# Kernel optimization log

Measured on AMD Instinct MI355X. Metric: run time of the kernel, lower is better.

The kernel has to match this reference:

```python
import jax, jax.numpy as jnp
import numpy as np

EMBED = 768
HEADS = 8
HEAD_DIM = EMBED // HEADS  # 96


def setup_inputs() -> dict:
    key = jax.random.key(0)
    k1, k2, k3, k4, k5 = jax.random.split(key, 5)
    b, n = 4, 2048
    x = jax.random.normal(k1, (b, n, EMBED), dtype=jnp.float32)
    s = 1.0 / np.sqrt(EMBED)
    W_qkv = jax.random.normal(k2, (EMBED, 3 * EMBED), dtype=jnp.float32) * s
    b_qkv = jax.random.normal(k3, (3 * EMBED,), dtype=jnp.float32) * 0.02
    W_proj = jax.random.normal(k4, (EMBED, EMBED), dtype=jnp.float32) * s
    b_proj = jax.random.normal(k5, (EMBED,), dtype=jnp.float32) * 0.02
    return {"x": x, "W_qkv": W_qkv, "b_qkv": b_qkv, "W_proj": W_proj, "b_proj": b_proj}


def reference(x, W_qkv, b_qkv, W_proj, b_proj):
    b, n, _ = x.shape
    qkv = x @ W_qkv + b_qkv  # [b, n, 3*EMBED]
    # rearrange 'b n (h d qkv) -> qkv b h n d': qkv is fastest-varying axis
    qkv = qkv.reshape(b, n, HEADS, HEAD_DIM, 3)
    q = jnp.transpose(qkv[..., 0], (0, 2, 1, 3))  # [b, h, n, d]
    k = jnp.transpose(qkv[..., 1], (0, 2, 1, 3))
    v = jnp.transpose(qkv[..., 2], (0, 2, 1, 3))
    scale = 1.0 / np.sqrt(HEAD_DIM)
    energy = jnp.einsum('bhqd,bhkd->bhqk', q, k) * scale
    attn = jax.nn.softmax(energy, axis=-1)  # dropout p=0 -> identity
    out = jnp.einsum('bhqk,bhkd->bhqd', attn, v)
    out = jnp.transpose(out, (0, 2, 1, 3)).reshape(b, n, EMBED)
    out = out @ W_proj + b_proj
    return out
```

## Files before the change

### kernel.cpp

```cpp
#include <hip/hip_runtime.h>
#include <hip/hip_bf16.h>

#define EMBED 768
#define NHEADS 8
#define HDIM 96
#define SEQ 2048
#define BATCH 4
#define NTOK (BATCH*SEQ)
#define QKVN (3*EMBED)

#define QSCALE 0.14724444f

typedef __attribute__((ext_vector_type(4))) float f32x4;
typedef __attribute__((ext_vector_type(8))) __bf16 bf16x8;

__device__ __forceinline__ unsigned short f2bf(float f) {
  union { float f; unsigned int u; } c; c.f = f;
  unsigned int u = c.u;
  return (unsigned short)((u + 0x7FFFu + ((u >> 16) & 1u)) >> 16);
}

__device__ __forceinline__ unsigned int cvt_pk_bf16(float lo, float hi) {
  unsigned int r;
  asm("v_cvt_pk_bf16_f32 %0, %1, %2" : "=v"(r) : "v"(lo), "v"(hi));
  return r;
}

__device__ __forceinline__ void gload_lds16(const void* g, void* l) {
  __builtin_amdgcn_global_load_lds(
      (const __attribute__((address_space(1))) unsigned int*)g,
      (__attribute__((address_space(3))) unsigned int*)l, 16, 0, 0);
}

__global__ __launch_bounds__(256) void cast_x_kernel(const float4* __restrict__ in,
                                                     ushort4* __restrict__ out, int n4) {
  int i = blockIdx.x * 256 + threadIdx.x;
  if (i >= n4) return;
  float4 v = in[i];
  out[i] = make_ushort4(f2bf(v.x), f2bf(v.y), f2bf(v.z), f2bf(v.w));
}

__global__ __launch_bounds__(256) void transpose_cast_kernel(const float* __restrict__ in,
                                                             unsigned short* __restrict__ out,
                                                             int R, int C, int remap) {
  __shared__ float t[32][33];
  int c0 = blockIdx.x * 32, r0 = blockIdx.y * 32;
  int tx = threadIdx.x & 31, ty = threadIdx.x >> 5;
  #pragma unroll
  for (int i = 0; i < 32; i += 8)
    t[ty + i][tx] = in[(size_t)(r0 + ty + i) * C + c0 + tx];
  __syncthreads();
  #pragma unroll
  for (int i = 0; i < 32; i += 8) {
    int c = c0 + ty + i;
    int rp = remap ? (c % 3) * 768 + c / 3 : c;
    out[(size_t)rp * R + r0 + tx] = f2bf(t[tx][ty + i]);
  }
}

template <int MODE>
__global__ __launch_bounds__(256, 2) void gemm8_kernel(
    const unsigned short* __restrict__ A, const unsigned short* __restrict__ B,
    const float* __restrict__ bias, int K, int NB,
    unsigned short* __restrict__ Qo, unsigned short* __restrict__ Ko,
    unsigned short* __restrict__ Vt, float* __restrict__ out) {
  __shared__ unsigned short As[2][128 * 64];
  __shared__ unsigned short Bs[2][128 * 64];
  const int tid = threadIdx.x;
  const int lane = tid & 63, wid = tid >> 6;
  const int wr = wid >> 1, wc = wid & 1;
  const int l15 = lane & 15, l16 = lane >> 4;
  const int cpx = gridDim.x >> 3;
  const int bid = blockIdx.x;
  const int swz = (bid & 7) * cpx + (bid >> 3);
  const int my = swz / NB, nx = swz - my * NB;
  const int m0 = my * 128, n0 = nx * 128;

  auto stage_half = [&](int buf, int kt, int half) {
    const unsigned short* src = half ? B : A;
    const int base0 = half ? n0 : m0;
    char* dst = (char*)(half ? &Bs[buf][0] : &As[buf][0]);
    #pragma unroll
    for (int i = 0; i < 4; i++) {
      int c = i * 256 + tid;
      int r = c >> 3, s = c & 7;
      gload_lds16(src + (size_t)(base0 + r) * K + kt * 64 + ((s ^ (r & 7)) << 3),
                  dst + (i * 256 + wid * 64) * 16);
    }
  };

  f32x4 acc[4][4] = {};
  const int xr = (l15 & 7) << 4;

  stage_half(0, 0, 0);
  stage_half(0, 0, 1);
  asm volatile("s_waitcnt vmcnt(0)" ::: "memory");
  __builtin_amdgcn_s_barrier();

  const int NT = K >> 6;
  for (int t = 0; t < NT; ++t) {
    const int cur = t & 1;
    const char* Ac = (const char*)&As[cur][0];
    const char* Bc = (const char*)&Bs[cur][0];
    #pragma unroll
    for (int kh = 0; kh < 2; ++kh) {
      bf16x8 af[4], bfr[4];
      #pragma unroll
      for (int mi = 0; mi < 4; mi++)
        af[mi] = *(const bf16x8*)(Ac + (wr * 64 + mi * 16 + l15) * 128 +
                                  ((kh * 64 + l16 * 16) ^ xr));
      #pragma unroll
      for (int ni = 0; ni < 4; ni++)
        bfr[ni] = *(const bf16x8*)(Bc + (wc * 64 + ni * 16 + l15) * 128 +
                                   ((kh * 64 + l16 * 16) ^ xr));
      if (t + 1 < NT) stage_half(cur ^ 1, t + 1, kh);
      __builtin_amdgcn_s_barrier();
      __builtin_amdgcn_s_setprio(1);
      #pragma unroll
      for (int mi = 0; mi < 4; mi++)
        #pragma unroll
        for (int ni = 0; ni < 4; ni++)
          acc[mi][ni] = __builtin_amdgcn_mfma_f32_16x16x32_bf16(af[mi], bfr[ni], acc[mi][ni], 0, 0, 0);
      __builtin_amdgcn_s_setprio(0);
      __builtin_amdgcn_s_barrier();
    }
    asm volatile("s_waitcnt lgkmcnt(0)" ::: "memory");
    asm volatile("s_waitcnt vmcnt(0)" ::: "memory");
    __builtin_amdgcn_sched_barrier(0);
    __builtin_amdgcn_s_barrier();
  }

  if (MODE == 0) {
    #pragma unroll
    for (int mi = 0; mi < 4; mi++) {
      #pragma unroll
      for (int ni = 0; ni < 4; ni++) {
        int base = n0 + wc * 64 + ni * 16;
        int which = base / 768;
        int hd = base - which * 768;
        int h = hd / 96;
        int d0 = hd - h * 96;
        float bb = bias[(hd + l15) * 3 + which];
        int rowb = m0 + wr * 64 + mi * 16 + l16 * 4;
        int bi = rowb >> 11, nnb = rowb & 2047;
        size_t bh = (size_t)(bi * NHEADS + h);
        if (which == 2) {
          int nn2 = (nnb & ~63) | (nnb & 32) | ((nnb & 12) << 1) | ((nnb & 16) >> 2) | (nnb & 3);
          float v0 = acc[mi][ni][0] + bb, v1 = acc[mi][ni][1] + bb;
          float v2 = acc[mi][ni][2] + bb, v3 = acc[mi][ni][3] + bb;
          uint2 pk;
          pk.x = cvt_pk_bf16(v0, v1);
          pk.y = cvt_pk_bf16(v2, v3);
          *(uint2*)(Vt + (bh * HDIM + d0 + l15) * SEQ + nn2) = pk;
        } else {
          #pragma unroll
          for (int j = 0; j < 4; j++) {
            float v = acc[mi][ni][j] + bb;
            int nn = nnb + j;
            if (which == 0) Qo[(bh * SEQ + nn) * HDIM + d0 + l15] = f2bf(v * QSCALE);
            else            Ko[(bh * SEQ + nn) * HDIM + d0 + l15] = f2bf(v);
          }
        }
      }
    }
  } else {
    #pragma unroll
    for (int mi = 0; mi < 4; mi++) {
      #pragma unroll
      for (int ni = 0; ni < 4; ni++) {
        int col = n0 + wc * 64 + ni * 16 + l15;
        float bb = bias[col];
        #pragma unroll
        for (int j = 0; j < 4; j++) {
          int row = m0 + wr * 64 + mi * 16 + l16 * 4 + j;
          out[(size_t)row * EMBED + col] = acc[mi][ni][j] + bb;
        }
      }
    }
  }
}

__global__ __launch_bounds__(512) void attn_kernel(
    const unsigned short* __restrict__ Q, const unsigned short* __restrict__ Kd,
    const unsigned short* __restrict__ Vt, unsigned short* __restrict__ Oa) {
  __shared__ unsigned short Ks[2][64 * 96];
  __shared__ unsigned short Vs[2][96 * 64];

  const int tid = threadIdx.x, lane = tid & 63, wid = tid >> 6;
  const int l15 = lane & 15, l16 = lane >> 4;
  const int bid = blockIdx.x;
  const int swz = (bid & 7) * 64 + (bid >> 3);
  const int qb_ = swz & 15, bh = swz >> 4;
  const int bi = bh >> 3, h = bh & 7;
  const int q0 = qb_ * 128;

  const unsigned short* Qg = Q + ((size_t)bh * SEQ + q0) * HDIM;
  const unsigned short* Kg = Kd + (size_t)bh * SEQ * HDIM;
  const unsigned short* Vg = Vt + (size_t)bh * HDIM * SEQ;

  bf16x8 qf[3];
  #pragma unroll
  for (int ks = 0; ks < 3; ks++)
    qf[ks] = *(const bf16x8*)(Qg + (size_t)(wid * 16 + l15) * HDIM + ks * 32 + l16 * 8);

  auto stageKV = [&](int buf, int k0) {
    gload_lds16(Kg + (size_t)k0 * HDIM + tid * 8, (char*)&Ks[buf][0] + wid * 1024);
    if (wid < 4)
      gload_lds16(Kg + (size_t)k0 * HDIM + (512 + tid) * 8,
                  (char*)&Ks[buf][0] + 8192 + wid * 1024);
    {
      int d = tid >> 3, s = tid & 7;
      gload_lds16(Vg + (size_t)d * SEQ + k0 + ((s ^ (d & 7)) << 3),
                  (char*)&Vs[buf][0] + wid * 1024);
    }
    if (wid < 4) {
      int idx = 512 + tid, d = idx >> 3, s = idx & 7;
      gload_lds16(Vg + (size_t)d * SEQ + k0 + ((s ^ (d & 7)) << 3),
                  (char*)&Vs[buf][0] + 8192 + wid * 1024);
    }
  };

  f32x4 oacc[6] = {};
  float mrow = -__builtin_inff(), lrow = 0.f;

  stageKV(0, 0);
  __syncthreads();

  for (int kb = 0; kb < SEQ / 64; kb++) {
    const int cur = kb & 1;
    if (kb + 1 < SEQ / 64) stageKV(cur ^ 1, (kb + 1) * 64);

    const char* Kc = (const char*)&Ks[cur][0];
    const char* Vc = (const char*)&Vs[cur][0];

    f32x4 sacc[4] = {};
    #pragma unroll
    for (int ks = 0; ks < 3; ks++) {
      bf16x8 ak[4];
      #pragma unroll
      for (int ni = 0; ni < 4; ni++)
        ak[ni] = *(const bf16x8*)(Kc + (ni * 16 + l15) * 192 + ks * 64 + l16 * 16);
      __builtin_amdgcn_s_setprio(1);
      #pragma unroll
      for (int ni = 0; ni < 4; ni++)
        sacc[ni] = __builtin_amdgcn_mfma_f32_16x16x32_bf16(ak[ni], qf[ks], sacc[ni], 0, 0, 0);
      __builtin_amdgcn_s_setprio(0);
    }

    float a0 = fmaxf(fmaxf(sacc[0][0], sacc[0][1]), fmaxf(sacc[0][2], sacc[0][3]));
    float a1 = fmaxf(fmaxf(sacc[1][0], sacc[1][1]), fmaxf(sacc[1][2], sacc[1][3]));
    float a2 = fmaxf(fmaxf(sacc[2][0], sacc[2][1]), fmaxf(sacc[2][2], sacc[2][3]));
    float a3 = fmaxf(fmaxf(sacc[3][0], sacc[3][1]), fmaxf(sacc[3][2], sacc[3][3]));
    float v = fmaxf(fmaxf(a0, a1), fmaxf(a2, a3));
    v = fmaxf(v, __shfl_xor(v, 16));
    v = fmaxf(v, __shfl_xor(v, 32));
    if (!__all(v - mrow <= 11.54f)) {
      float mnew = fmaxf(mrow, v);
      float alpha = __builtin_amdgcn_exp2f(mrow - mnew);
      mrow = mnew;
      lrow *= alpha;
      #pragma unroll
      for (int d6 = 0; d6 < 6; d6++) {
        oacc[d6][0] *= alpha; oacc[d6][1] *= alpha;
        oacc[d6][2] *= alpha; oacc[d6][3] *= alpha;
      }
    }

    unsigned int pk[8];
    {
      float psum = 0.f;
      #pragma unroll
      for (int ni = 0; ni < 4; ni++) {
        float p0 = __builtin_amdgcn_exp2f(sacc[ni][0] - mrow);
        float p1 = __builtin_amdgcn_exp2f(sacc[ni][1] - mrow);
        float p2 = __builtin_amdgcn_exp2f(sacc[ni][2] - mrow);
        float p3 = __builtin_amdgcn_exp2f(sacc[ni][3] - mrow);
        psum += (p0 + p1) + (p2 + p3);
        pk[ni * 2]     = cvt_pk_bf16(p0, p1);
        pk[ni * 2 + 1] = cvt_pk_bf16(p2, p3);
      }
      psum += __shfl_xor(psum, 16);
      psum += __shfl_xor(psum, 32);
      lrow += psum;
    }

    #pragma unroll
    for (int ks = 0; ks < 2; ks++) {
      bf16x8 vb[6];
      #pragma unroll
      for (int d6 = 0; d6 < 6; d6++)
        vb[d6] = *(const bf16x8*)(Vc + (d6 * 16 + l15) * 128 +
                                  (((ks * 4 + l16) ^ (l15 & 7)) << 4));
      union { unsigned int u[4]; bf16x8 v; } pf;
      pf.u[0] = pk[4 * ks];     pf.u[1] = pk[4 * ks + 1];
      pf.u[2] = pk[4 * ks + 2]; pf.u[3] = pk[4 * ks + 3];
      __builtin_amdgcn_s_setprio(1);
      #pragma unroll
      for (int d6 = 0; d6 < 6; d6++)
        oacc[d6] = __builtin_amdgcn_mfma_f32_16x16x32_bf16(vb[d6], pf.v, oacc[d6], 0, 0, 0);
      __builtin_amdgcn_s_setprio(0);
    }

    __syncthreads();
  }

  {
    const float rl = 1.f / lrow;
    const int tok = q0 + wid * 16 + l15;
    unsigned short* Og = Oa + ((size_t)bi * SEQ + tok) * EMBED + h * HDIM;
    #pragma unroll
    for (int d6 = 0; d6 < 6; d6++) {
      uint2 o;
      o.x = cvt_pk_bf16(oacc[d6][0] * rl, oacc[d6][1] * rl);
      o.y = cvt_pk_bf16(oacc[d6][2] * rl, oacc[d6][3] * rl);
      *(uint2*)(Og + d6 * 16 + l16 * 4) = o;
    }
  }
}

extern "C" void kernel_launch(void* const* d_in, const int* in_sizes, int n_in,
                              void* d_out, int out_size, void* d_ws, size_t ws_size,
                              hipStream_t stream) {
  const float* x      = (const float*)d_in[0];
  const float* W_qkv  = (const float*)d_in[1];
  const float* b_qkv  = (const float*)d_in[2];
  const float* W_proj = (const float*)d_in[3];
  const float* b_proj = (const float*)d_in[4];
  float* out = (float*)d_out;

  char* ws = (char*)d_ws;
  size_t off = 0;
  auto alloc = [&](size_t bytes) { void* p = ws + off; off += (bytes + 255) & ~(size_t)255; return p; };
  unsigned short* xb  = (unsigned short*)alloc((size_t)NTOK * EMBED * 2);
  unsigned short* WqT = (unsigned short*)alloc((size_t)QKVN * EMBED * 2);
  unsigned short* WpT = (unsigned short*)alloc((size_t)EMBED * EMBED * 2);
  unsigned short* Qb  = (unsigned short*)alloc((size_t)NTOK * EMBED * 2);
  unsigned short* Kb  = (unsigned short*)alloc((size_t)NTOK * EMBED * 2);
  unsigned short* Vtb = (unsigned short*)alloc((size_t)NTOK * EMBED * 2);
  unsigned short* Ob  = (unsigned short*)alloc((size_t)NTOK * EMBED * 2);

  cast_x_kernel<<<dim3(NTOK * EMBED / 4 / 256), dim3(256), 0, stream>>>(
      (const float4*)x, (ushort4*)xb, NTOK * EMBED / 4);
  transpose_cast_kernel<<<dim3(QKVN / 32, EMBED / 32), dim3(256), 0, stream>>>(W_qkv, WqT, EMBED, QKVN, 1);
  transpose_cast_kernel<<<dim3(EMBED / 32, EMBED / 32), dim3(256), 0, stream>>>(W_proj, WpT, EMBED, EMBED, 0);

  gemm8_kernel<0><<<dim3((NTOK / 128) * (QKVN / 128)), dim3(256), 0, stream>>>(
      xb, WqT, b_qkv, EMBED, QKVN / 128, Qb, Kb, Vtb, nullptr);

  attn_kernel<<<dim3(BATCH * NHEADS * (SEQ / 128)), dim3(512), 0, stream>>>(Qb, Kb, Vtb, Ob);

  gemm8_kernel<1><<<dim3((NTOK / 128) * (EMBED / 128)), dim3(256), 0, stream>>>(
      Ob, WpT, b_proj, EMBED, EMBED / 128, nullptr, nullptr, nullptr, out);
}
```

Measured before the change: 159.2 us.

## Switch attention to 32x32x16 MFMA with 4 waves of 32 query rows

Rewrites the attention inner loop to use 32x32x16 bf16 MFMA instead of 16x16x32. Each wave now owns 32 query rows, so blocks shrink to 256 threads. The K LDS layout becomes a k-chunk-major arrangement, and the V token permutation in the QKV GEMM epilogue changes to match the new P fragment layout. The aim is fewer MFMA issues and LDS fragment reads per flop, plus a cheaper row reduction, at the cost of higher register pressure (f32x16 accumulators) and fewer waves per block.

```diff
diff --git a/kernel.cpp b/kernel.cpp
--- a/kernel.cpp
+++ b/kernel.cpp
@@ -12,6 +12,7 @@
 #define QSCALE 0.14724444f
 
 typedef __attribute__((ext_vector_type(4))) float f32x4;
+typedef __attribute__((ext_vector_type(16))) float f32x16;
 typedef __attribute__((ext_vector_type(8))) __bf16 bf16x8;
 
 __device__ __forceinline__ unsigned short f2bf(float f) {
@@ -145,7 +146,7 @@
         int bi = rowb >> 11, nnb = rowb & 2047;
         size_t bh = (size_t)(bi * NHEADS + h);
         if (which == 2) {
-          int nn2 = (nnb & ~63) | (nnb & 32) | ((nnb & 12) << 1) | ((nnb & 16) >> 2) | (nnb & 3);
+          int nn2 = (nnb & ~12) | ((nnb & 4) << 1) | ((nnb & 8) >> 1);
           float v0 = acc[mi][ni][0] + bb, v1 = acc[mi][ni][1] + bb;
           float v2 = acc[mi][ni][2] + bb, v3 = acc[mi][ni][3] + bb;
           uint2 pk;
@@ -180,14 +181,14 @@
   }
 }
 
-__global__ __launch_bounds__(512) void attn_kernel(
+__global__ __launch_bounds__(256) void attn_kernel(
     const unsigned short* __restrict__ Q, const unsigned short* __restrict__ Kd,
     const unsigned short* __restrict__ Vt, unsigned short* __restrict__ Oa) {
   __shared__ unsigned short Ks[2][64 * 96];
   __shared__ unsigned short Vs[2][96 * 64];
 
   const int tid = threadIdx.x, lane = tid & 63, wid = tid >> 6;
-  const int l15 = lane & 15, l16 = lane >> 4;
+  const int l31 = lane & 31, hi = lane >> 5;
   const int bid = blockIdx.x;
   const int swz = (bid & 7) * 64 + (bid >> 3);
   const int qb_ = swz & 15, bh = swz >> 4;
@@ -198,29 +199,29 @@
   const unsigned short* Kg = Kd + (size_t)bh * SEQ * HDIM;
   const unsigned short* Vg = Vt + (size_t)bh * HDIM * SEQ;
 
-  bf16x8 qf[3];
+  bf16x8 qf[6];
   #pragma unroll
-  for (int ks = 0; ks < 3; ks++)
-    qf[ks] = *(const bf16x8*)(Qg + (size_t)(wid * 16 + l15) * HDIM + ks * 32 + l16 * 8);
+  for (int ks = 0; ks < 6; ks++)
+    qf[ks] = *(const bf16x8*)(Qg + (size_t)(wid * 32 + l31) * HDIM + ks * 16 + hi * 8);
 
   auto stageKV = [&](int buf, int k0) {
-    gload_lds16(Kg + (size_t)k0 * HDIM + tid * 8, (char*)&Ks[buf][0] + wid * 1024);
-    if (wid < 4)
-      gload_lds16(Kg + (size_t)k0 * HDIM + (512 + tid) * 8,
-                  (char*)&Ks[buf][0] + 8192 + wid * 1024);
-    {
-      int d = tid >> 3, s = tid & 7;
+    #pragma unroll
+    for (int i = 0; i < 3; i++) {
+      int g = i * 256 + tid;
+      int o = g >> 6, kv = g & 63;
+      gload_lds16(Kg + (size_t)(k0 + kv) * HDIM + o * 8,
+                  (char*)&Ks[buf][0] + (i * 256 + wid * 64) * 16);
+    }
+    #pragma unroll
+    for (int i = 0; i < 3; i++) {
+      int idx = i * 256 + tid;
+      int d = idx >> 3, s = idx & 7;
       gload_lds16(Vg + (size_t)d * SEQ + k0 + ((s ^ (d & 7)) << 3),
-                  (char*)&Vs[buf][0] + wid * 1024);
-    }
-    if (wid < 4) {
-      int idx = 512 + tid, d = idx >> 3, s = idx & 7;
-      gload_lds16(Vg + (size_t)d * SEQ + k0 + ((s ^ (d & 7)) << 3),
-                  (char*)&Vs[buf][0] + 8192 + wid * 1024);
+                  (char*)&Vs[buf][0] + (i * 256 + wid * 64) * 16);
     }
   };
 
-  f32x4 oacc[6] = {};
+  f32x16 oacc[3] = {};
   float mrow = -__builtin_inff(), lrow = 0.f;
 
   stageKV(0, 0);
@@ -233,26 +234,21 @@
     const char* Kc = (const char*)&Ks[cur][0];
     const char* Vc = (const char*)&Vs[cur][0];
 
-    f32x4 sacc[4] = {};
-    #pragma unroll
-    for (int ks = 0; ks < 3; ks++) {
-      bf16x8 ak[4];
-      #pragma unroll
-      for (int ni = 0; ni < 4; ni++)
-        ak[ni] = *(const bf16x8*)(Kc + (ni * 16 + l15) * 192 + ks * 64 + l16 * 16);
+    f32x16 sacc[2] = {};
+    #pragma unroll
+    for (int ks = 0; ks < 6; ks++) {
+      bf16x8 ak0 = *(const bf16x8*)(Kc + (((2 * ks + hi) * 64) + l31) * 16);
+      bf16x8 ak1 = *(const bf16x8*)(Kc + (((2 * ks + hi) * 64) + 32 + l31) * 16);
       __builtin_amdgcn_s_setprio(1);
-      #pragma unroll
-      for (int ni = 0; ni < 4; ni++)
-        sacc[ni] = __builtin_amdgcn_mfma_f32_16x16x32_bf16(ak[ni], qf[ks], sacc[ni], 0, 0, 0);
+      sacc[0] = __builtin_amdgcn_mfma_f32_32x32x16_bf16(ak0, qf[ks], sacc[0], 0, 0, 0);
+      sacc[1] = __builtin_amdgcn_mfma_f32_32x32x16_bf16(ak1, qf[ks], sacc[1], 0, 0, 0);
       __builtin_amdgcn_s_setprio(0);
     }
 
-    float a0 = fmaxf(fmaxf(sacc[0][0], sacc[0][1]), fmaxf(sacc[0][2], sacc[0][3]));
-    float a1 = fmaxf(fmaxf(sacc[1][0], sacc[1][1]), fmaxf(sacc[1][2], sacc[1][3]));
-    float a2 = fmaxf(fmaxf(sacc[2][0], sacc[2][1]), fmaxf(sacc[2][2], sacc[2][3]));
-    float a3 = fmaxf(fmaxf(sacc[3][0], sacc[3][1]), fmaxf(sacc[3][2], sacc[3][3]));
-    float v = fmaxf(fmaxf(a0, a1), fmaxf(a2, a3));
-    v = fmaxf(v, __shfl_xor(v, 16));
+    float v = fmaxf(sacc[0][0], sacc[1][0]);
+    #pragma unroll
+    for (int r = 1; r < 16; r++)
+      v = fmaxf(v, fmaxf(sacc[0][r], sacc[1][r]));
     v = fmaxf(v, __shfl_xor(v, 32));
     if (!__all(v - mrow <= 11.54f)) {
       float mnew = fmaxf(mrow, v);
@@ -260,61 +256,60 @@
       mrow = mnew;
       lrow *= alpha;
       #pragma unroll
-      for (int d6 = 0; d6 < 6; d6++) {
-        oacc[d6][0] *= alpha; oacc[d6][1] *= alpha;
-        oacc[d6][2] *= alpha; oacc[d6][3] *= alpha;
-      }
-    }
-
-    unsigned int pk[8];
-    {
-      float psum = 0.f;
-      #pragma unroll
-      for (int ni = 0; ni < 4; ni++) {
-        float p0 = __builtin_amdgcn_exp2f(sacc[ni][0] - mrow);
-        float p1 = __builtin_amdgcn_exp2f(sacc[ni][1] - mrow);
-        float p2 = __builtin_amdgcn_exp2f(sacc[ni][2] - mrow);
-        float p3 = __builtin_amdgcn_exp2f(sacc[ni][3] - mrow);
-        psum += (p0 + p1) + (p2 + p3);
-        pk[ni * 2]     = cvt_pk_bf16(p0, p1);
-        pk[ni * 2 + 1] = cvt_pk_bf16(p2, p3);
-      }
-      psum += __shfl_xor(psum, 16);
-      psum += __shfl_xor(psum, 32);
-      lrow += psum;
-    }
-
-    #pragma unroll
-    for (int ks = 0; ks < 2; ks++) {
-      bf16x8 vb[6];
-      #pragma unroll
-      for (int d6 = 0; d6 < 6; d6++)
-        vb[d6] = *(const bf16x8*)(Vc + (d6 * 16 + l15) * 128 +
-                                  (((ks * 4 + l16) ^ (l15 & 7)) << 4));
-      union { unsigned int u[4]; bf16x8 v; } pf;
-      pf.u[0] = pk[4 * ks];     pf.u[1] = pk[4 * ks + 1];
-      pf.u[2] = pk[4 * ks + 2]; pf.u[3] = pk[4 * ks + 3];
-      __builtin_amdgcn_s_setprio(1);
-      #pragma unroll
-      for (int d6 = 0; d6 < 6; d6++)
-        oacc[d6] = __builtin_amdgcn_mfma_f32_16x16x32_bf16(vb[d6], pf.v, oacc[d6], 0, 0, 0);
-      __builtin_amdgcn_s_setprio(0);
-    }
+      for (int db = 0; db < 3; db++)
+        #pragma unroll
+        for (int r = 0; r < 16; r++)
+          oacc[db][r] *= alpha;
+    }
+
+    unsigned int pk[2][8];
+    float psum = 0.f;
+    #pragma unroll
+    for (int kbk = 0; kbk < 2; kbk++)
+      #pragma unroll
+      for (int j2 = 0; j2 < 8; j2++) {
+        float p0 = __builtin_amdgcn_exp2f(sacc[kbk][2 * j2] - mrow);
+        float p1 = __builtin_amdgcn_exp2f(sacc[kbk][2 * j2 + 1] - mrow);
+        psum += p0 + p1;
+        pk[kbk][j2] = cvt_pk_bf16(p0, p1);
+      }
+    psum += __shfl_xor(psum, 32);
+    lrow += psum;
+
+    #pragma unroll
+    for (int kbk = 0; kbk < 2; kbk++)
+      #pragma unroll
+      for (int t = 0; t < 2; t++) {
+        union { unsigned int u[4]; bf16x8 v; } pf;
+        pf.u[0] = pk[kbk][4 * t];     pf.u[1] = pk[kbk][4 * t + 1];
+        pf.u[2] = pk[kbk][4 * t + 2]; pf.u[3] = pk[kbk][4 * t + 3];
+        const int sidx = (kbk * 2 + t) * 2 + hi;
+        __builtin_amdgcn_s_setprio(1);
+        #pragma unroll
+        for (int db = 0; db < 3; db++) {
+          int d = db * 32 + l31;
+          bf16x8 vb = *(const bf16x8*)(Vc + d * 128 + ((sidx ^ (d & 7)) << 4));
+          oacc[db] = __builtin_amdgcn_mfma_f32_32x32x16_bf16(vb, pf.v, oacc[db], 0, 0, 0);
+        }
+        __builtin_amdgcn_s_setprio(0);
+      }
 
     __syncthreads();
   }
 
   {
     const float rl = 1.f / lrow;
-    const int tok = q0 + wid * 16 + l15;
+    const int tok = q0 + wid * 32 + l31;
     unsigned short* Og = Oa + ((size_t)bi * SEQ + tok) * EMBED + h * HDIM;
     #pragma unroll
-    for (int d6 = 0; d6 < 6; d6++) {
-      uint2 o;
-      o.x = cvt_pk_bf16(oacc[d6][0] * rl, oacc[d6][1] * rl);
-      o.y = cvt_pk_bf16(oacc[d6][2] * rl, oacc[d6][3] * rl);
-      *(uint2*)(Og + d6 * 16 + l16 * 4) = o;
-    }
+    for (int db = 0; db < 3; db++)
+      #pragma unroll
+      for (int rq = 0; rq < 4; rq++) {
+        uint2 o;
+        o.x = cvt_pk_bf16(oacc[db][4 * rq] * rl, oacc[db][4 * rq + 1] * rl);
+        o.y = cvt_pk_bf16(oacc[db][4 * rq + 2] * rl, oacc[db][4 * rq + 3] * rl);
+        *(uint2*)(Og + db * 32 + rq * 8 + hi * 4) = o;
+      }
   }
 }
 
@@ -347,7 +342,7 @@
   gemm8_kernel<0><<<dim3((NTOK / 128) * (QKVN / 128)), dim3(256), 0, stream>>>(
       xb, WqT, b_qkv, EMBED, QKVN / 128, Qb, Kb, Vtb, nullptr);
 
-  attn_kernel<<<dim3(BATCH * NHEADS * (SEQ / 128)), dim3(512), 0, stream>>>(Qb, Kb, Vtb, Ob);
+  attn_kernel<<<dim3(BATCH * NHEADS * (SEQ / 128)), dim3(256), 0, stream>>>(Qb, Kb, Vtb, Ob);
 
   gemm8_kernel<1><<<dim3((NTOK / 128) * (EMBED / 128)), dim3(256), 0, stream>>>(
       Ob, WpT, b_proj, EMBED, EMBED / 128, nullptr, nullptr, nullptr, out);
```

Result: no change. 158.1 us (-0.7%).
